# Kernel optimization log

Measured on AMD Instinct MI355X. Metric: run time of the kernel, lower is better.

## Reference

```python
import jax, jax.numpy as jnp
import numpy as np
import math

N_HEADS = 16
D_EMBED = 1024
D_HEAD = D_EMBED // N_HEADS


def setup_inputs() -> dict:
    key = jax.random.key(0)
    ks = jax.random.split(key, 5)
    B, T = 4, 2048
    x = jax.random.normal(ks[0], (B, T, D_EMBED), dtype=jnp.float32)
    s_in = 1.0 / math.sqrt(D_EMBED)
    W_in = jax.random.normal(ks[1], (3 * D_EMBED, D_EMBED), dtype=jnp.float32) * s_in
    b_in = jax.random.normal(ks[2], (3 * D_EMBED,), dtype=jnp.float32) * s_in
    W_out = jax.random.normal(ks[3], (D_EMBED, D_EMBED), dtype=jnp.float32) * s_in
    b_out = jax.random.normal(ks[4], (D_EMBED,), dtype=jnp.float32) * s_in
    return {"x": x, "W_in": W_in, "b_in": b_in, "W_out": W_out, "b_out": b_out,
            "causal_mask": 1}


def reference(x, W_in, b_in, W_out, b_out, causal_mask):
    B, T, C = x.shape
    # in_proj: x @ W_in^T + b_in -> (B,T,3C), chunk into q,k,v
    qkv = jnp.einsum('btc,ec->bte', x, W_in) + b_in
    q, k, v = jnp.split(qkv, 3, axis=-1)
    # (B,T,H,Dh) -> (B,H,T,Dh)
    def heads(t):
        return t.reshape(B, T, N_HEADS, D_HEAD).transpose(0, 2, 1, 3)
    q, k, v = heads(q), heads(k), heads(v)
    scores = jnp.einsum('bhqd,bhkd->bhqk', q, k) / math.sqrt(D_HEAD)
    if causal_mask:
        mask = jnp.triu(jnp.ones((T, T), dtype=bool), k=1)  # True above diagonal
        scores = jnp.where(mask, -jnp.inf, scores)
    attn = jax.nn.softmax(scores, axis=-1)
    out = jnp.einsum('bhqk,bhkd->bhqd', attn, v)
    out = out.transpose(0, 2, 1, 3).reshape(B, T, C)
    out = jnp.einsum('btc,oc->bto', out, W_out) + b_out
    return out
```

## Files before the change

### kernel.cpp

```cpp
#include <hip/hip_runtime.h>
#include <hip/hip_bf16.h>

#define T_SEQ 2048
#define D_EMB 1024
#define NH    16
#define DH    64
#define NB    4
#define MROWS (NB * T_SEQ)
#define QKVN  (3 * D_EMB)

typedef __attribute__((ext_vector_type(8))) short bf16x8;
typedef __attribute__((ext_vector_type(4))) float f32x4;

__device__ __forceinline__ unsigned short f2bf(float f) {
  __hip_bfloat16 h = __float2bfloat16(f);
  return __builtin_bit_cast(unsigned short, h);
}

__device__ __forceinline__ void gload_lds16(const void* g, void* lds) {
  __builtin_amdgcn_global_load_lds(
      (const __attribute__((address_space(1))) void*)g,
      (__attribute__((address_space(3))) void*)lds, 16, 0, 0);
}

__device__ __forceinline__ float redmax16(float v) {
  v = fmaxf(v, __shfl_xor(v, 1));
  v = fmaxf(v, __shfl_xor(v, 2));
  v = fmaxf(v, __shfl_xor(v, 4));
  v = fmaxf(v, __shfl_xor(v, 8));
  return v;
}
__device__ __forceinline__ float redsum16(float v) {
  v += __shfl_xor(v, 1);
  v += __shfl_xor(v, 2);
  v += __shfl_xor(v, 4);
  v += __shfl_xor(v, 8);
  return v;
}

__global__ __launch_bounds__(256) void cvt_kernel(const float* __restrict__ in,
                                                  unsigned short* __restrict__ out,
                                                  int n4) {
  for (int i = blockIdx.x * 256 + threadIdx.x; i < n4; i += gridDim.x * 256) {
    const float4 v = reinterpret_cast<const float4*>(in)[i];
    ushort4 o;
    o.x = f2bf(v.x); o.y = f2bf(v.y); o.z = f2bf(v.z); o.w = f2bf(v.w);
    reinterpret_cast<ushort4*>(out)[i] = o;
  }
}

template <int OUT_BF16>
__global__ __launch_bounds__(256) void gemm_bt(const unsigned short* __restrict__ A,
                                               const unsigned short* __restrict__ Bt,
                                               const float* __restrict__ bias,
                                               void* __restrict__ Cout,
                                               int M, int N, int K) {
  __shared__ __align__(16) unsigned short As[128 * 32];
  __shared__ __align__(16) unsigned short Bs[128 * 32];

  const int tid = threadIdx.x;
  const int w  = tid >> 6;
  const int l  = tid & 63;
  const int lr = l & 15;
  const int lk = (l >> 4) * 8;
  const int bm = blockIdx.y * 128;
  const int bn = blockIdx.x * 128;
  const int wr = (w >> 1) * 64;
  const int wc = (w & 1) * 64;

  f32x4 acc[4][4];
#pragma unroll
  for (int i = 0; i < 4; ++i)
#pragma unroll
    for (int j = 0; j < 4; ++j) acc[i][j] = (f32x4){0.f, 0.f, 0.f, 0.f};

  const int srow = l >> 2;
  const int sk   = (l & 3) * 8;
  const unsigned short* Ab = A + (size_t)(bm + w * 32 + srow) * K + sk;
  const unsigned short* Bb = Bt + (size_t)(bn + w * 32 + srow) * K + sk;

  for (int kt = 0; kt < K; kt += 32) {
    gload_lds16(Ab + kt,                  &As[(w * 32 + 0) * 32]);
    gload_lds16(Ab + kt + (size_t)16 * K, &As[(w * 32 + 16) * 32]);
    gload_lds16(Bb + kt,                  &Bs[(w * 32 + 0) * 32]);
    gload_lds16(Bb + kt + (size_t)16 * K, &Bs[(w * 32 + 16) * 32]);
    __syncthreads();

    bf16x8 a[4], b[4];
#pragma unroll
    for (int mi = 0; mi < 4; ++mi)
      a[mi] = *reinterpret_cast<const bf16x8*>(&As[(wr + mi * 16 + lr) * 32 + lk]);
#pragma unroll
    for (int ni = 0; ni < 4; ++ni)
      b[ni] = *reinterpret_cast<const bf16x8*>(&Bs[(wc + ni * 16 + lr) * 32 + lk]);
#pragma unroll
    for (int mi = 0; mi < 4; ++mi)
#pragma unroll
      for (int ni = 0; ni < 4; ++ni)
        acc[mi][ni] = __builtin_amdgcn_mfma_f32_16x16x32_bf16(a[mi], b[ni], acc[mi][ni], 0, 0, 0);
    __syncthreads();
  }

  const int lg = l >> 4;
#pragma unroll
  for (int mi = 0; mi < 4; ++mi)
#pragma unroll
    for (int ni = 0; ni < 4; ++ni)
#pragma unroll
      for (int i = 0; i < 4; ++i) {
        const int row = bm + wr + mi * 16 + lg * 4 + i;
        const int col = bn + wc + ni * 16 + lr;
        const float v = acc[mi][ni][i] + bias[col];
        if (OUT_BF16)
          ((unsigned short*)Cout)[(size_t)row * N + col] = f2bf(v);
        else
          ((float*)Cout)[(size_t)row * N + col] = v;
      }
}

__global__ __launch_bounds__(512, 4) void attn_fwd(const unsigned short* __restrict__ qkv,
                                                   unsigned short* __restrict__ attn_out,
                                                   const int* __restrict__ causal_flag) {
  __shared__ __align__(16) unsigned short Ks[64 * 64];
  __shared__ __align__(16) unsigned short Vt[64 * 64];
  __shared__ __align__(16) unsigned short Ps[8][16 * 64];

  const int tid = threadIdx.x;
  const int w  = tid >> 6;
  const int l  = tid & 63;
  const int lr = l & 15;
  const int lg = l >> 4;
  const int lk = lg * 8;
  const int bx = blockIdx.x;
  const int bh = blockIdx.y;
  const int b  = bh >> 4;
  const int h  = bh & 15;
  const int causal = causal_flag[0];

  const unsigned short* Qp = qkv + (size_t)(b * T_SEQ) * QKVN + h * DH;
  const unsigned short* Kp = Qp + D_EMB;
  const unsigned short* Vp = Qp + 2 * D_EMB;

  for (int qq = 0; qq < 2; ++qq) {
    const int qt = qq ? (15 - bx) : bx;
    const int qbase = qt * 128;
    const int wrow0 = qbase + w * 16;

    bf16x8 qf[2];
#pragma unroll
    for (int ks = 0; ks < 2; ++ks) {
      bf16x8 v = *reinterpret_cast<const bf16x8*>(
          Qp + (size_t)(wrow0 + lr) * QKVN + ks * 32 + lk);
#pragma unroll
      for (int j = 0; j < 8; ++j) {
        const float f = __builtin_bit_cast(float, ((unsigned)(unsigned short)v[j]) << 16) * 0.125f;
        v[j] = (short)(__builtin_bit_cast(unsigned, f) >> 16);
      }
      qf[ks] = v;
    }

    f32x4 oacc[4];
    float mrow[4], lsum[4];
#pragma unroll
    for (int di = 0; di < 4; ++di) oacc[di] = (f32x4){0.f, 0.f, 0.f, 0.f};
#pragma unroll
    for (int i = 0; i < 4; ++i) { mrow[i] = -INFINITY; lsum[i] = 0.f; }

    const int nt = causal ? (qt * 2 + 2) : (T_SEQ / 64);

    for (int kb = 0; kb < nt; ++kb) {
      const int kbase = kb * 64;
      {
        const int cj = (l & 7) ^ (l >> 3);
        gload_lds16(Kp + (size_t)(kbase + w * 8 + (l >> 3)) * QKVN + cj * 8,
                    &Ks[(w * 8) * 64]);
      }
      {
        const int k  = tid & 63;
        const int d0 = (tid >> 6) * 8;
        bf16x8 v = *reinterpret_cast<const bf16x8*>(Vp + (size_t)(kbase + k) * QKVN + d0);
#pragma unroll
        for (int j = 0; j < 8; ++j)
          Vt[(d0 + j) * 64 + (k ^ (j << 3))] = ((unsigned short*)&v)[j];
      }
      __syncthreads();

      const bool live = !causal || (kbase <= wrow0 + 15);
      if (live) {
        f32x4 s[4];
#pragma unroll
        for (int ni = 0; ni < 4; ++ni) s[ni] = (f32x4){0.f, 0.f, 0.f, 0.f};
#pragma unroll
        for (int ks = 0; ks < 2; ++ks) {
          bf16x8 kf[4];
#pragma unroll
          for (int ni = 0; ni < 4; ++ni) {
            const int R = ni * 16 + lr;
            kf[ni] = *reinterpret_cast<const bf16x8*>(
                &Ks[R * 64 + (((ks * 4 + lg) ^ (lr & 7)) << 3)]);
          }
#pragma unroll
          for (int ni = 0; ni < 4; ++ni)
            s[ni] = __builtin_amdgcn_mfma_f32_16x16x32_bf16(qf[ks], kf[ni], s[ni], 0, 0, 0);
        }

        const bool mm = causal && (kbase + 63 > wrow0);
#pragma unroll
        for (int i = 0; i < 4; ++i) {
          const int qrow = wrow0 + lg * 4 + i;
          float rmax = -INFINITY;
#pragma unroll
          for (int ni = 0; ni < 4; ++ni) {
            float v = s[ni][i];
            if (mm && (kbase + ni * 16 + lr > qrow)) v = -INFINITY;
            s[ni][i] = v;
            rmax = fmaxf(rmax, v);
          }
          rmax = redmax16(rmax);
          const float mnew = fmaxf(mrow[i], rmax);
          const float alpha = __expf(mrow[i] - mnew);
          mrow[i] = mnew;
          float psum = 0.f;
#pragma unroll
          for (int ni = 0; ni < 4; ++ni) {
            const float p = __expf(s[ni][i] - mnew);
            s[ni][i] = p;
            psum += p;
          }
          psum = redsum16(psum);
          lsum[i] = lsum[i] * alpha + psum;
#pragma unroll
          for (int di = 0; di < 4; ++di) oacc[di][i] *= alpha;
          const int rp = lg * 4 + i;
#pragma unroll
          for (int ni = 0; ni < 4; ++ni)
            Ps[w][rp * 64 + ((ni * 16 + lr) ^ ((rp & 7) << 3))] = f2bf(s[ni][i]);
        }

#pragma unroll
        for (int ks2 = 0; ks2 < 2; ++ks2) {
          bf16x8 pf, vf[4];
          pf = *reinterpret_cast<const bf16x8*>(
              &Ps[w][lr * 64 + (((ks2 * 4 + lg) ^ (lr & 7)) << 3)]);
#pragma unroll
          for (int di = 0; di < 4; ++di) {
            const int R = di * 16 + lr;
            vf[di] = *reinterpret_cast<const bf16x8*>(
                &Vt[R * 64 + (((ks2 * 4 + lg) ^ (lr & 7)) << 3)]);
          }
#pragma unroll
          for (int di = 0; di < 4; ++di)
            oacc[di] = __builtin_amdgcn_mfma_f32_16x16x32_bf16(pf, vf[di], oacc[di], 0, 0, 0);
        }
      }
      __syncthreads();
    }

#pragma unroll
    for (int i = 0; i < 4; ++i) {
      const float inv = 1.0f / lsum[i];
#pragma unroll
      for (int di = 0; di < 4; ++di) {
        const int q = wrow0 + lg * 4 + i;
        const int d = di * 16 + lr;
        attn_out[(size_t)(b * T_SEQ + q) * D_EMB + h * DH + d] =
            f2bf(oacc[di][i] * inv);
      }
    }
  }
}

extern "C" void kernel_launch(void* const* d_in, const int* in_sizes, int n_in,
                              void* d_out, int out_size, void* d_ws, size_t ws_size,
                              hipStream_t stream) {
  const float* x     = (const float*)d_in[0];
  const float* W_in  = (const float*)d_in[1];
  const float* b_in  = (const float*)d_in[2];
  const float* W_out = (const float*)d_in[3];
  const float* b_out = (const float*)d_in[4];
  const int*   causal = (const int*)d_in[5];
  float* out = (float*)d_out;

  char* ws = (char*)d_ws;
  unsigned short* x_bf    = (unsigned short*)(ws);
  unsigned short* win_bf  = (unsigned short*)(ws + 16777216);
  unsigned short* wout_bf = (unsigned short*)(ws + 23068672);
  unsigned short* qkv     = (unsigned short*)(ws + 25165824);
  unsigned short* attn    = (unsigned short*)(ws + 75497472);

  cvt_kernel<<<2048, 256, 0, stream>>>(x, x_bf, (MROWS * D_EMB) / 4);
  cvt_kernel<<<2048, 256, 0, stream>>>(W_in, win_bf, (QKVN * D_EMB) / 4);
  cvt_kernel<<<1024, 256, 0, stream>>>(W_out, wout_bf, (D_EMB * D_EMB) / 4);

  gemm_bt<1><<<dim3(QKVN / 128, MROWS / 128), 256, 0, stream>>>(
      x_bf, win_bf, b_in, qkv, MROWS, QKVN, D_EMB);

  attn_fwd<<<dim3(8, NB * NH), 512, 0, stream>>>(qkv, attn, causal);

  gemm_bt<0><<<dim3(D_EMB / 128, MROWS / 128), 256, 0, stream>>>(
      attn, wout_bf, b_out, out, MROWS, D_EMB, D_EMB);
}
```

Baseline: 322.5 us.

## Double-buffer K/V tiles in attention to overlap global loads with compute

Splits the K and V shared-memory tiles into two buffers so each iteration prefetches the next tile while computing on the current one. K goes through async global-to-LDS loads and V is held in registers and transposed into LDS after compute. This hides global memory latency behind the MFMA work. It costs double the LDS for K/V, which may lower occupancy, adds register pressure, and keeps two barriers per iteration.

```diff
diff --git a/kernel.cpp b/kernel.cpp
--- a/kernel.cpp
+++ b/kernel.cpp
@@ -121,8 +121,8 @@
 __global__ __launch_bounds__(512, 4) void attn_fwd(const unsigned short* __restrict__ qkv,
                                                    unsigned short* __restrict__ attn_out,
                                                    const int* __restrict__ causal_flag) {
-  __shared__ __align__(16) unsigned short Ks[64 * 64];
-  __shared__ __align__(16) unsigned short Vt[64 * 64];
+  __shared__ __align__(16) unsigned short Ks[2][64 * 64];
+  __shared__ __align__(16) unsigned short Vt[2][64 * 64];
   __shared__ __align__(16) unsigned short Ps[8][16 * 64];
 
   const int tid = threadIdx.x;
@@ -141,6 +141,11 @@
   const unsigned short* Kp = Qp + D_EMB;
   const unsigned short* Vp = Qp + 2 * D_EMB;
 
+  const int scj = (l & 7) ^ (l >> 3);
+  const int skr = w * 8 + (l >> 3);
+  const int svk = tid & 63;
+  const int svd = (tid >> 6) * 8;
+
   for (int qq = 0; qq < 2; ++qq) {
     const int qt = qq ? (15 - bx) : bx;
     const int qbase = qt * 128;
@@ -168,22 +173,25 @@
 
     const int nt = causal ? (qt * 2 + 2) : (T_SEQ / 64);
 
+    gload_lds16(Kp + (size_t)skr * QKVN + scj * 8, &Ks[0][(w * 8) * 64]);
+    bf16x8 vreg = *reinterpret_cast<const bf16x8*>(Vp + (size_t)svk * QKVN + svd);
+#pragma unroll
+    for (int j = 0; j < 8; ++j)
+      Vt[0][(svd + j) * 64 + (svk ^ (j << 3))] = ((unsigned short*)&vreg)[j];
+    __syncthreads();
+
     for (int kb = 0; kb < nt; ++kb) {
+      const int buf = kb & 1, nb = buf ^ 1;
       const int kbase = kb * 64;
-      {
-        const int cj = (l & 7) ^ (l >> 3);
-        gload_lds16(Kp + (size_t)(kbase + w * 8 + (l >> 3)) * QKVN + cj * 8,
-                    &Ks[(w * 8) * 64]);
-      }
-      {
-        const int k  = tid & 63;
-        const int d0 = (tid >> 6) * 8;
-        bf16x8 v = *reinterpret_cast<const bf16x8*>(Vp + (size_t)(kbase + k) * QKVN + d0);
-#pragma unroll
-        for (int j = 0; j < 8; ++j)
-          Vt[(d0 + j) * 64 + (k ^ (j << 3))] = ((unsigned short*)&v)[j];
-      }
-      __syncthreads();
+      const bool pre = (kb + 1 < nt);
+
+      if (pre) {
+        const int nkbase = kbase + 64;
+        gload_lds16(Kp + (size_t)(nkbase + skr) * QKVN + scj * 8,
+                    &Ks[nb][(w * 8) * 64]);
+        vreg = *reinterpret_cast<const bf16x8*>(
+            Vp + (size_t)(nkbase + svk) * QKVN + svd);
+      }
 
       const bool live = !causal || (kbase <= wrow0 + 15);
       if (live) {
@@ -197,7 +205,7 @@
           for (int ni = 0; ni < 4; ++ni) {
             const int R = ni * 16 + lr;
             kf[ni] = *reinterpret_cast<const bf16x8*>(
-                &Ks[R * 64 + (((ks * 4 + lg) ^ (lr & 7)) << 3)]);
+                &Ks[buf][R * 64 + (((ks * 4 + lg) ^ (lr & 7)) << 3)]);
           }
 #pragma unroll
           for (int ni = 0; ni < 4; ++ni)
@@ -246,12 +254,19 @@
           for (int di = 0; di < 4; ++di) {
             const int R = di * 16 + lr;
             vf[di] = *reinterpret_cast<const bf16x8*>(
-                &Vt[R * 64 + (((ks2 * 4 + lg) ^ (lr & 7)) << 3)]);
+                &Vt[buf][R * 64 + (((ks2 * 4 + lg) ^ (lr & 7)) << 3)]);
           }
 #pragma unroll
           for (int di = 0; di < 4; ++di)
             oacc[di] = __builtin_amdgcn_mfma_f32_16x16x32_bf16(pf, vf[di], oacc[di], 0, 0, 0);
         }
+      }
+
+      __syncthreads();
+      if (pre) {
+#pragma unroll
+        for (int j = 0; j < 8; ++j)
+          Vt[nb][(svd + j) * 64 + (svk ^ (j << 3))] = ((unsigned short*)&vreg)[j];
       }
       __syncthreads();
     }
```

Result: slower. 330.5 us (+2.5%).

## Transpose QK^T MFMA so each lane owns a query row in softmax

Applied to the files above, without the earlier changes.

Swaps the MFMA operand order so the score tile is transposed, giving each lane a single query row across 16 key values. Row max and sum then need only two cross-lane shuffles per tile instead of four shuffles per row for four rows, and the running max and sum become scalars. The softmax scale is folded with log2(e) so exp2f replaces __expf. P is written to LDS as packed 8-byte stores, and alpha and lsum are broadcast back to the output-accumulator layout with __shfl, which adds some shuffle traffic in exchange.

```diff
diff --git a/kernel.cpp b/kernel.cpp
--- a/kernel.cpp
+++ b/kernel.cpp
@@ -21,21 +21,6 @@
   __builtin_amdgcn_global_load_lds(
       (const __attribute__((address_space(1))) void*)g,
       (__attribute__((address_space(3))) void*)lds, 16, 0, 0);
-}
-
-__device__ __forceinline__ float redmax16(float v) {
-  v = fmaxf(v, __shfl_xor(v, 1));
-  v = fmaxf(v, __shfl_xor(v, 2));
-  v = fmaxf(v, __shfl_xor(v, 4));
-  v = fmaxf(v, __shfl_xor(v, 8));
-  return v;
-}
-__device__ __forceinline__ float redsum16(float v) {
-  v += __shfl_xor(v, 1);
-  v += __shfl_xor(v, 2);
-  v += __shfl_xor(v, 4);
-  v += __shfl_xor(v, 8);
-  return v;
 }
 
 __global__ __launch_bounds__(256) void cvt_kernel(const float* __restrict__ in,
@@ -153,18 +138,17 @@
           Qp + (size_t)(wrow0 + lr) * QKVN + ks * 32 + lk);
 #pragma unroll
       for (int j = 0; j < 8; ++j) {
-        const float f = __builtin_bit_cast(float, ((unsigned)(unsigned short)v[j]) << 16) * 0.125f;
+        const float f = __builtin_bit_cast(float, ((unsigned)(unsigned short)v[j]) << 16)
+                        * 0.180336879f;
         v[j] = (short)(__builtin_bit_cast(unsigned, f) >> 16);
       }
       qf[ks] = v;
     }
 
     f32x4 oacc[4];
-    float mrow[4], lsum[4];
+    float mrow = -INFINITY, lsum = 0.f;
 #pragma unroll
     for (int di = 0; di < 4; ++di) oacc[di] = (f32x4){0.f, 0.f, 0.f, 0.f};
-#pragma unroll
-    for (int i = 0; i < 4; ++i) { mrow[i] = -INFINITY; lsum[i] = 0.f; }
 
     const int nt = causal ? (qt * 2 + 2) : (T_SEQ / 64);
 
@@ -201,40 +185,54 @@
           }
 #pragma unroll
           for (int ni = 0; ni < 4; ++ni)
-            s[ni] = __builtin_amdgcn_mfma_f32_16x16x32_bf16(qf[ks], kf[ni], s[ni], 0, 0, 0);
+            s[ni] = __builtin_amdgcn_mfma_f32_16x16x32_bf16(kf[ni], qf[ks], s[ni], 0, 0, 0);
         }
 
         const bool mm = causal && (kbase + 63 > wrow0);
-#pragma unroll
-        for (int i = 0; i < 4; ++i) {
-          const int qrow = wrow0 + lg * 4 + i;
-          float rmax = -INFINITY;
-#pragma unroll
-          for (int ni = 0; ni < 4; ++ni) {
+        const int qrow_rel = wrow0 + lr - kbase;
+        float rmax = -INFINITY;
+#pragma unroll
+        for (int ni = 0; ni < 4; ++ni)
+#pragma unroll
+          for (int i = 0; i < 4; ++i) {
             float v = s[ni][i];
-            if (mm && (kbase + ni * 16 + lr > qrow)) v = -INFINITY;
+            if (mm && (ni * 16 + lg * 4 + i > qrow_rel)) v = -INFINITY;
             s[ni][i] = v;
             rmax = fmaxf(rmax, v);
           }
-          rmax = redmax16(rmax);
-          const float mnew = fmaxf(mrow[i], rmax);
-          const float alpha = __expf(mrow[i] - mnew);
-          mrow[i] = mnew;
-          float psum = 0.f;
-#pragma unroll
-          for (int ni = 0; ni < 4; ++ni) {
-            const float p = __expf(s[ni][i] - mnew);
+        rmax = fmaxf(rmax, __shfl_xor(rmax, 16));
+        rmax = fmaxf(rmax, __shfl_xor(rmax, 32));
+        const float mnew = fmaxf(mrow, rmax);
+        const float alpha = exp2f(mrow - mnew);
+        mrow = mnew;
+        float psum = 0.f;
+#pragma unroll
+        for (int ni = 0; ni < 4; ++ni)
+#pragma unroll
+          for (int i = 0; i < 4; ++i) {
+            const float p = exp2f(s[ni][i] - mnew);
             s[ni][i] = p;
             psum += p;
           }
-          psum = redsum16(psum);
-          lsum[i] = lsum[i] * alpha + psum;
-#pragma unroll
-          for (int di = 0; di < 4; ++di) oacc[di][i] *= alpha;
-          const int rp = lg * 4 + i;
-#pragma unroll
-          for (int ni = 0; ni < 4; ++ni)
-            Ps[w][rp * 64 + ((ni * 16 + lr) ^ ((rp & 7) << 3))] = f2bf(s[ni][i]);
+        psum += __shfl_xor(psum, 16);
+        psum += __shfl_xor(psum, 32);
+        lsum = lsum * alpha + psum;
+
+#pragma unroll
+        for (int i = 0; i < 4; ++i) {
+          const float a_bc = __shfl(alpha, (l & 48) | (lg * 4 + i));
+#pragma unroll
+          for (int di = 0; di < 4; ++di) oacc[di][i] *= a_bc;
+        }
+
+#pragma unroll
+        for (int ni = 0; ni < 4; ++ni) {
+          const unsigned lo = (unsigned)f2bf(s[ni][0]) | ((unsigned)f2bf(s[ni][1]) << 16);
+          const unsigned hi = (unsigned)f2bf(s[ni][2]) | ((unsigned)f2bf(s[ni][3]) << 16);
+          const int chunk = (ni * 2 + (lg >> 1)) ^ (lr & 7);
+          uint2* dst = reinterpret_cast<uint2*>(
+              reinterpret_cast<char*>(&Ps[w][0]) + lr * 128 + chunk * 16 + (lg & 1) * 8);
+          *dst = make_uint2(lo, hi);
         }
 
 #pragma unroll
@@ -258,7 +256,8 @@
 
 #pragma unroll
     for (int i = 0; i < 4; ++i) {
-      const float inv = 1.0f / lsum[i];
+      const float ls = __shfl(lsum, (l & 48) | (lg * 4 + i));
+      const float inv = 1.0f / ls;
 #pragma unroll
       for (int di = 0; di < 4; ++di) {
         const int q = wrow0 + lg * 4 + i;
```

Measured after the change: 299.2 us. 1.08x faster.
